# Performance work log

Measured on AMD Instinct MI355X. Metric: run time of the kernel, lower is better.

Reference implementation:

```python
import jax, jax.numpy as jnp
import numpy as np

EPS = 1e-06


def setup_inputs() -> dict:
    key = jax.random.key(0)
    k1, k2, k3 = jax.random.split(key, 3)
    L, B, H, D = 4096, 4, 8, 64
    Q = jax.random.normal(k1, (L, B, H, D), dtype=jnp.float32)
    K = jax.random.normal(k2, (L, B, H, D), dtype=jnp.float32)
    V = jax.random.normal(k3, (L, B, H, D), dtype=jnp.float32)
    return {"Q": Q, "K": K, "V": V}


def reference(Q, K, V):
    # feature map: elu(x) + 1 (positive features)
    phiQ = jax.nn.elu(Q) + 1.0  # [L, B, H, D]
    phiK = jax.nn.elu(K) + 1.0  # [L, B, H, D]
    # Associative rewrite of sum_k phiK_k (x) V_k : per-(batch,head) KV state [D, Dv]
    kv = jnp.einsum('lbhd,lbhe->bhde', phiK, V)          # [B, H, D, Dv]
    num = jnp.einsum('lbhd,bhde->lbhe', phiQ, kv)        # [L, B, H, Dv]
    ksum = jnp.sum(phiK, axis=0)                          # [B, H, D]
    den = jnp.einsum('lbhd,bhd->lbh', phiQ, ksum)[..., None]  # [L, B, H, 1]
    return num / (den + EPS)
```

## Files before the change

kernel.cpp:

```cpp
#include <hip/hip_runtime.h>
#include <math.h>


#define L_TOT 4096
#define NBH   32
#define ROWSTRIDE 2048
#define KVSZ  4160
#define EPS_  1e-6f

typedef short s16x8 __attribute__((ext_vector_type(8)));
typedef float f32x4 __attribute__((ext_vector_type(4)));

union FragU { unsigned int u[4]; s16x8 s; };

__device__ __forceinline__ float phi_(float x) {
    return x > 0.0f ? x + 1.0f : __expf(x);
}

__device__ __forceinline__ unsigned int bf16rn_(float x) {
    unsigned int u = __float_as_uint(x);
    return (u + 0x7FFFu + ((u >> 16) & 1u)) >> 16;
}

__device__ __forceinline__ s16x8 frag_from_(const unsigned short* p) {
    uint2 a = *(const uint2*)p;
    uint2 b = *(const uint2*)(p + 4);
    FragU f;
    f.u[0] = a.x; f.u[1] = a.y; f.u[2] = b.x; f.u[3] = b.y;
    return f.s;
}

__global__ __launch_bounds__(256) void kv_partial_kernel(
    const float* __restrict__ K, const float* __restrict__ V,
    float* __restrict__ part, int Lc)
{
    __shared__ __align__(16) unsigned short kphi[64][36];
    __shared__ __align__(16) unsigned short vtr [64][36];

    const int tid  = threadIdx.x;
    const int w    = tid >> 6;
    const int lane = tid & 63;
    const int c    = blockIdx.x;
    const int bh   = blockIdx.y;
    const int l0c  = c * Lc;
    const int ntiles = Lc >> 5;

    const int sr = tid >> 4;
    const int sc = (tid & 15) * 4;
    const size_t bh_off = (size_t)bh * 64;

    const int ar = lane & 15;
    const int ag = lane >> 4;

    f32x4 acc[4];
    f32x4 aks = {0.f, 0.f, 0.f, 0.f};
    #pragma unroll
    for (int n = 0; n < 4; ++n) { f32x4 z = {0.f,0.f,0.f,0.f}; acc[n] = z; }

    FragU onesU;
    #pragma unroll
    for (int p = 0; p < 4; ++p) onesU.u[p] = 0x3F803F80u;
    const s16x8 ones = onesU.s;

    size_t gb = (size_t)(l0c + sr) * ROWSTRIDE + bh_off + sc;
    float4 ka = *(const float4*)(K + gb);
    float4 va = *(const float4*)(V + gb);
    float4 kb = *(const float4*)(K + gb + 16 * ROWSTRIDE);
    float4 vb = *(const float4*)(V + gb + 16 * ROWSTRIDE);

    for (int t = 0; t < ntiles; ++t) {
        {
            float kx[4] = {ka.x, ka.y, ka.z, ka.w};
            float vx[4] = {va.x, va.y, va.z, va.w};
            float ky[4] = {kb.x, kb.y, kb.z, kb.w};
            float vy[4] = {vb.x, vb.y, vb.z, vb.w};
            #pragma unroll
            for (int i = 0; i < 4; ++i) {
                kphi[sc + i][sr]      = (unsigned short)bf16rn_(phi_(kx[i]));
                kphi[sc + i][sr + 16] = (unsigned short)bf16rn_(phi_(ky[i]));
                vtr [sc + i][sr]      = (unsigned short)bf16rn_(vx[i]);
                vtr [sc + i][sr + 16] = (unsigned short)bf16rn_(vy[i]);
            }
        }
        __syncthreads();

        if (t + 1 < ntiles) {
            gb = (size_t)(l0c + (t + 1) * 32 + sr) * ROWSTRIDE + bh_off + sc;
            ka = *(const float4*)(K + gb);
            va = *(const float4*)(V + gb);
            kb = *(const float4*)(K + gb + 16 * ROWSTRIDE);
            vb = *(const float4*)(V + gb + 16 * ROWSTRIDE);
        }

        const s16x8 afrag = frag_from_(&kphi[w * 16 + ar][ag * 8]);

        #pragma unroll
        for (int nt = 0; nt < 4; ++nt) {
            const s16x8 bfrag = frag_from_(&vtr[nt * 16 + ar][ag * 8]);
            acc[nt] = __builtin_amdgcn_mfma_f32_16x16x32_bf16(afrag, bfrag, acc[nt], 0, 0, 0);
        }
        aks = __builtin_amdgcn_mfma_f32_16x16x32_bf16(afrag, ones, aks, 0, 0, 0);

        __syncthreads();
    }

    float* pb = part + ((size_t)c * NBH + bh) * KVSZ;
    #pragma unroll
    for (int nt = 0; nt < 4; ++nt) {
        #pragma unroll
        for (int r = 0; r < 4; ++r) {
            const int d_row = w * 16 + (lane >> 4) * 4 + r;
            const int e_col = nt * 16 + (lane & 15);
            pb[d_row * 64 + e_col] = acc[nt][r];
        }
    }
    if ((lane & 15) == 0) {
        #pragma unroll
        for (int r = 0; r < 4; ++r)
            pb[4096 + w * 16 + (lane >> 4) * 4 + r] = aks[r];
    }
}

__global__ __launch_bounds__(256) void kv_reduce_kernel(
    const float* __restrict__ part, float* __restrict__ fin, int nchunk)
{
    const int i4 = blockIdx.x * 256 + threadIdx.x;
    if (i4 >= (NBH * KVSZ) / 4) return;
    const int slab4 = KVSZ / 4;
    const int bh = i4 / slab4;
    const int r  = (i4 - bh * slab4) * 4;

    float4 s = make_float4(0.f, 0.f, 0.f, 0.f);
    for (int cc = 0; cc < nchunk; ++cc) {
        const float4 v = *(const float4*)(part + ((size_t)cc * NBH + bh) * KVSZ + r);
        s.x += v.x; s.y += v.y; s.z += v.z; s.w += v.w;
    }
    float* fb = fin + (size_t)bh * KVSZ;
    if (r < 4096) {
        const int d = r >> 6;
        const int e = r & 63;
        fb[(e + 0) * 64 + d] = s.x;
        fb[(e + 1) * 64 + d] = s.y;
        fb[(e + 2) * 64 + d] = s.z;
        fb[(e + 3) * 64 + d] = s.w;
    } else {
        fb[r + 0] = s.x; fb[r + 1] = s.y; fb[r + 2] = s.z; fb[r + 3] = s.w;
    }
}

__global__ __launch_bounds__(512) void attn_out_kernel(
    const float* __restrict__ Q, const float* __restrict__ fin,
    float* __restrict__ out)
{
    __shared__ __align__(16) unsigned short khi[80 * 72];
    __shared__ __align__(16) unsigned short klo[80 * 72];

    const int tid  = threadIdx.x;
    const int lane = tid & 63;
    const int w    = tid >> 6;
    const int bh   = blockIdx.x & 31;
    const int tg   = blockIdx.x >> 5;
    const int wt0  = tg * 256 + w * 32;

    const float* __restrict__ fb = fin + (size_t)bh * KVSZ;

    for (int idx = tid; idx < 2080; idx += 512) {
        const int e = idx >> 5;
        const int p = idx & 31;
        const float2 x2 = *(const float2*)(fb + e * 64 + 2 * p);
        unsigned int u0 = __float_as_uint(x2.x), u1 = __float_as_uint(x2.y);
        unsigned int hi = (u1 & 0xFFFF0000u) | (u0 >> 16);
        float r0 = x2.x - __uint_as_float(u0 & 0xFFFF0000u);
        float r1 = x2.y - __uint_as_float(u1 & 0xFFFF0000u);
        unsigned int lo = (bf16rn_(r1) << 16) | bf16rn_(r0);
        ((unsigned int*)(khi + e * 72))[p] = hi;
        ((unsigned int*)(klo + e * 72))[p] = lo;
    }
    for (int idx = tid; idx < 480; idx += 512) {
        const int e = 65 + (idx >> 5);
        const int p = idx & 31;
        ((unsigned int*)(khi + e * 72))[p] = 0u;
        ((unsigned int*)(klo + e * 72))[p] = 0u;
    }

    const int arow = lane & 15;
    const int agrp = lane >> 4;
    s16x8 ahi[2][2];
    #pragma unroll
    for (int m = 0; m < 2; ++m) {
        #pragma unroll
        for (int kc = 0; kc < 2; ++kc) {
            const float* qp = Q + (size_t)(wt0 + m*16 + arow) * ROWSTRIDE
                                + (size_t)bh * 64 + kc*32 + agrp*8;
            float4 qa = *(const float4*)qp;
            float4 qb = *(const float4*)(qp + 4);
            float x[8] = {qa.x,qa.y,qa.z,qa.w,qb.x,qb.y,qb.z,qb.w};
            FragU fh;
            #pragma unroll
            for (int p = 0; p < 4; ++p) {
                float p0 = phi_(x[2*p]), p1 = phi_(x[2*p+1]);
                fh.u[p] = (bf16rn_(p1) << 16) | bf16rn_(p0);
            }
            ahi[m][kc] = fh.s;
        }
    }
    __syncthreads();

    f32x4 acc[2][5];
    #pragma unroll
    for (int m = 0; m < 2; ++m) {
        #pragma unroll
        for (int n = 0; n < 5; ++n) { f32x4 z = {0.f,0.f,0.f,0.f}; acc[m][n] = z; }
    }

    #pragma unroll
    for (int nt = 0; nt < 5; ++nt) {
        #pragma unroll
        for (int kc = 0; kc < 2; ++kc) {
            const int off = (nt*16 + arow) * 72 + kc*32 + agrp*8;
            s16x8 bh_ = *(const s16x8*)(khi + off);
            s16x8 bl_ = *(const s16x8*)(klo + off);
            #pragma unroll
            for (int m = 0; m < 2; ++m) {
                acc[m][nt] = __builtin_amdgcn_mfma_f32_16x16x32_bf16(ahi[m][kc], bh_, acc[m][nt], 0, 0, 0);
                acc[m][nt] = __builtin_amdgcn_mfma_f32_16x16x32_bf16(ahi[m][kc], bl_, acc[m][nt], 0, 0, 0);
            }
        }
    }

    const int baddr = (lane & 48) << 2;
    float inv[2][4];
    #pragma unroll
    for (int m = 0; m < 2; ++m) {
        #pragma unroll
        for (int r = 0; r < 4; ++r) {
            float dv = __int_as_float(
                __builtin_amdgcn_ds_bpermute(baddr, __float_as_int(acc[m][4][r])));
            inv[m][r] = 1.0f / (dv + EPS_);
        }
    }

    #pragma unroll
    for (int m = 0; m < 2; ++m) {
        #pragma unroll
        for (int r = 0; r < 4; ++r) {
            const int t = wt0 + m*16 + (lane >> 4) * 4 + r;
            float* op = out + (size_t)t * ROWSTRIDE + (size_t)bh * 64 + (lane & 15);
            #pragma unroll
            for (int nt = 0; nt < 4; ++nt)
                op[nt * 16] = acc[m][nt][r] * inv[m][r];
        }
    }
}

extern "C" void kernel_launch(void* const* d_in, const int* in_sizes, int n_in,
                              void* d_out, int out_size, void* d_ws, size_t ws_size,
                              hipStream_t stream) {
    const float* Q = (const float*)d_in[0];
    const float* K = (const float*)d_in[1];
    const float* V = (const float*)d_in[2];
    float* outp = (float*)d_out;
    float* ws   = (float*)d_ws;

    const size_t slab = (size_t)NBH * KVSZ;
    const size_t cap  = ws_size / (slab * sizeof(float));

    int nchunk = 1;
    {
        const int cand[4] = {16, 8, 4, 2};
        for (int i = 0; i < 4; ++i) {
            if (cap >= (size_t)cand[i] + 1) { nchunk = cand[i]; break; }
        }
    }
    const int Lc = L_TOT / nchunk;

    float* fin  = ws;
    float* part = ws + slab;

    hipLaunchKernelGGL(kv_partial_kernel, dim3(nchunk, NBH), dim3(256), 0, stream,
                       K, V, part, Lc);
    {
        const int nb = ((NBH * KVSZ) / 4 + 255) / 256;
        hipLaunchKernelGGL(kv_reduce_kernel, dim3(nb), dim3(256), 0, stream,
                           part, fin, nchunk);
    }
    hipLaunchKernelGGL(attn_out_kernel, dim3(512), dim3(512), 0, stream,
                       Q, fin, outp);
}
```

Baseline: 38.44 us.

## Fuse chunk reduction into output kernel and transpose partials via LDS

```diff
diff --git a/kernel.cpp b/kernel.cpp
--- a/kernel.cpp
+++ b/kernel.cpp
@@ -34,8 +34,9 @@
     const float* __restrict__ K, const float* __restrict__ V,
     float* __restrict__ part, int Lc)
 {
-    __shared__ __align__(16) unsigned short kphi[64][36];
-    __shared__ __align__(16) unsigned short vtr [64][36];
+    __shared__ __align__(16) unsigned short kphi[64][40];
+    __shared__ __align__(16) unsigned short vtr [64][40];
+    __shared__ __align__(16) float xpose[64 * 65];
 
     const int tid  = threadIdx.x;
     const int w    = tid >> 6;
@@ -104,15 +105,27 @@
         __syncthreads();
     }
 
-    float* pb = part + ((size_t)c * NBH + bh) * KVSZ;
     #pragma unroll
     for (int nt = 0; nt < 4; ++nt) {
         #pragma unroll
         for (int r = 0; r < 4; ++r) {
             const int d_row = w * 16 + (lane >> 4) * 4 + r;
             const int e_col = nt * 16 + (lane & 15);
-            pb[d_row * 64 + e_col] = acc[nt][r];
-        }
+            xpose[d_row * 65 + e_col] = acc[nt][r];
+        }
+    }
+    __syncthreads();
+
+    float* pb = part + ((size_t)c * NBH + bh) * KVSZ;
+    for (int u = tid; u < 1024; u += 256) {
+        const int e  = u >> 4;
+        const int jj = u & 15;
+        float4 o;
+        o.x = xpose[(4 * jj + 0) * 65 + e];
+        o.y = xpose[(4 * jj + 1) * 65 + e];
+        o.z = xpose[(4 * jj + 2) * 65 + e];
+        o.w = xpose[(4 * jj + 3) * 65 + e];
+        *(float4*)&pb[e * 64 + 4 * jj] = o;
     }
     if ((lane & 15) == 0) {
         #pragma unroll
@@ -121,36 +134,9 @@
     }
 }
 
-__global__ __launch_bounds__(256) void kv_reduce_kernel(
-    const float* __restrict__ part, float* __restrict__ fin, int nchunk)
-{
-    const int i4 = blockIdx.x * 256 + threadIdx.x;
-    if (i4 >= (NBH * KVSZ) / 4) return;
-    const int slab4 = KVSZ / 4;
-    const int bh = i4 / slab4;
-    const int r  = (i4 - bh * slab4) * 4;
-
-    float4 s = make_float4(0.f, 0.f, 0.f, 0.f);
-    for (int cc = 0; cc < nchunk; ++cc) {
-        const float4 v = *(const float4*)(part + ((size_t)cc * NBH + bh) * KVSZ + r);
-        s.x += v.x; s.y += v.y; s.z += v.z; s.w += v.w;
-    }
-    float* fb = fin + (size_t)bh * KVSZ;
-    if (r < 4096) {
-        const int d = r >> 6;
-        const int e = r & 63;
-        fb[(e + 0) * 64 + d] = s.x;
-        fb[(e + 1) * 64 + d] = s.y;
-        fb[(e + 2) * 64 + d] = s.z;
-        fb[(e + 3) * 64 + d] = s.w;
-    } else {
-        fb[r + 0] = s.x; fb[r + 1] = s.y; fb[r + 2] = s.z; fb[r + 3] = s.w;
-    }
-}
-
 __global__ __launch_bounds__(512) void attn_out_kernel(
-    const float* __restrict__ Q, const float* __restrict__ fin,
-    float* __restrict__ out)
+    const float* __restrict__ Q, const float* __restrict__ part,
+    float* __restrict__ out, int nchunk)
 {
     __shared__ __align__(16) unsigned short khi[80 * 72];
     __shared__ __align__(16) unsigned short klo[80 * 72];
@@ -162,16 +148,19 @@
     const int tg   = blockIdx.x >> 5;
     const int wt0  = tg * 256 + w * 32;
 
-    const float* __restrict__ fb = fin + (size_t)bh * KVSZ;
-
     for (int idx = tid; idx < 2080; idx += 512) {
         const int e = idx >> 5;
         const int p = idx & 31;
-        const float2 x2 = *(const float2*)(fb + e * 64 + 2 * p);
-        unsigned int u0 = __float_as_uint(x2.x), u1 = __float_as_uint(x2.y);
+        float sx = 0.f, sy = 0.f;
+        for (int cc = 0; cc < nchunk; ++cc) {
+            const float2 v = *(const float2*)(part
+                + ((size_t)cc * NBH + bh) * KVSZ + e * 64 + 2 * p);
+            sx += v.x; sy += v.y;
+        }
+        unsigned int u0 = __float_as_uint(sx), u1 = __float_as_uint(sy);
         unsigned int hi = (u1 & 0xFFFF0000u) | (u0 >> 16);
-        float r0 = x2.x - __uint_as_float(u0 & 0xFFFF0000u);
-        float r1 = x2.y - __uint_as_float(u1 & 0xFFFF0000u);
+        float r0 = sx - __uint_as_float(u0 & 0xFFFF0000u);
+        float r1 = sy - __uint_as_float(u1 & 0xFFFF0000u);
         unsigned int lo = (bf16rn_(r1) << 16) | bf16rn_(r0);
         ((unsigned int*)(khi + e * 72))[p] = hi;
         ((unsigned int*)(klo + e * 72))[p] = lo;
@@ -260,30 +249,22 @@
     const float* K = (const float*)d_in[1];
     const float* V = (const float*)d_in[2];
     float* outp = (float*)d_out;
-    float* ws   = (float*)d_ws;
+    float* part = (float*)d_ws;
 
     const size_t slab = (size_t)NBH * KVSZ;
-    const size_t cap  = ws_size / (slab * sizeof(float));
 
     int nchunk = 1;
     {
+        const size_t cap = ws_size / (slab * sizeof(float));
         const int cand[4] = {16, 8, 4, 2};
         for (int i = 0; i < 4; ++i) {
-            if (cap >= (size_t)cand[i] + 1) { nchunk = cand[i]; break; }
+            if (cap >= (size_t)cand[i]) { nchunk = cand[i]; break; }
         }
     }
     const int Lc = L_TOT / nchunk;
-
-    float* fin  = ws;
-    float* part = ws + slab;
 
     hipLaunchKernelGGL(kv_partial_kernel, dim3(nchunk, NBH), dim3(256), 0, stream,
                        K, V, part, Lc);
-    {
-        const int nb = ((NBH * KVSZ) / 4 + 255) / 256;
-        hipLaunchKernelGGL(kv_reduce_kernel, dim3(nb), dim3(256), 0, stream,
-                           part, fin, nchunk);
-    }
     hipLaunchKernelGGL(attn_out_kernel, dim3(512), dim3(512), 0, stream,
-                       Q, fin, outp);
-}
+                       Q, part, outp, nchunk);
+}
```

Result: slower. 52.97 us (+37.8%).
